# Performance work log

Measured on AMD Instinct MI355X. Metric: run time of the kernel, lower is better.

The kernel has to match this reference:

```python
import jax, jax.numpy as jnp
import numpy as np

STRIDES = (8.0, 16.0, 32.0)
SCORE_T = 0.25
NMS_T = 0.45
DET = 100          # max detections per image
PRE_NMS = 1000     # static top-k surrogate for torch.where score filtering
MAX_SIZE = 4096.0  # class offset for batched (class-aware) NMS
IMG = 640.0        # image side (square), used for box clamping
ANCHORS = np.array([[[10,13],[16,30],[33,23]],
                    [[30,61],[62,45],[59,119]],
                    [[116,90],[156,198],[373,326]]], dtype=np.float32)


def setup_inputs() -> dict:
    key = jax.random.key(0)
    k0, k1, k2 = jax.random.split(key, 3)
    return {
        "pred0": jax.random.normal(k0, (16, 80, 80, 3, 85), dtype=jnp.float32),
        "pred1": jax.random.normal(k1, (16, 40, 40, 3, 85), dtype=jnp.float32),
        "pred2": jax.random.normal(k2, (16, 20, 20, 3, 85), dtype=jnp.float32),
        "anchors": jnp.asarray(ANCHORS),
        "scale_factors": jnp.ones((16,), dtype=jnp.float32),
    }


def _decode_level(pred, stride, anc):
    # pred: [B,H,W,A,5+C], anc: [A,2]
    p = jax.nn.sigmoid(pred)
    B, H, W, A, E = p.shape
    C = E - 5
    gx, gy = jnp.meshgrid(jnp.arange(W, dtype=p.dtype),
                          jnp.arange(H, dtype=p.dtype), indexing='xy')
    grid = jnp.stack((gx, gy), -1)                      # [H,W,2] = (x,y)
    xy = (2.0 * p[..., :2] - 0.5 + grid[None, :, :, None, :]) * stride
    wh = 4.0 * jnp.square(p[..., 2:4]) * anc            # [B,H,W,A,2]
    boxes = jnp.concatenate((xy - wh * 0.5, xy + wh * 0.5), -1)  # cxcywh->xyxy
    obj = p[..., 4:5]
    s = obj * p[..., 5:]                                # [B,H,W,A,C]
    s = jnp.where((obj > SCORE_T) & (s > SCORE_T), s, 0.0)
    return boxes.reshape(B, -1, 4), s.reshape(B, -1, C)


def _box_iou_1n(box, boxes):
    # box [4], boxes [K,4] -> iou [K]
    lt = jnp.maximum(box[:2], boxes[:, :2])
    rb = jnp.minimum(box[2:], boxes[:, 2:])
    wh = jnp.clip(rb - lt, 0.0)
    inter = wh[:, 0] * wh[:, 1]
    a1 = (box[2] - box[0]) * (box[3] - box[1])
    a2 = (boxes[:, 2] - boxes[:, 0]) * (boxes[:, 3] - boxes[:, 1])
    return inter / (a1 + a2 - inter + 1e-7)


def _per_image(boxes, scores, scale):
    # boxes [M,4], scores [M,C]
    C = scores.shape[-1]
    topv, topi = jax.lax.top_k(scores.reshape(-1), PRE_NMS)
    bidx = topi // C
    lab = topi % C
    bx = boxes[bidx]                                    # [K,4]
    obx = bx + lab.astype(bx.dtype)[:, None] * MAX_SIZE  # class-offset boxes

    def body(i, st):
        sc, keep, ks = st
        j = jnp.argmax(sc)
        keep = keep.at[i].set(j)
        ks = ks.at[i].set(sc[j])
        iou = _box_iou_1n(obx[j], obx)
        sc = jnp.where(iou > NMS_T, 0.0, sc)
        return sc, keep, ks

    st0 = (topv, jnp.zeros((DET,), jnp.int32), jnp.zeros((DET,), bx.dtype))
    _, keep, ks = jax.lax.fori_loop(0, DET, body, st0)
    kb = bx[keep] / scale
    kl = lab[keep].astype(bx.dtype)
    valid = ks > 0
    kb = jnp.where(valid[:, None], kb, 0.0)
    kl = jnp.where(valid, kl, -1.0)
    return jnp.concatenate((kb, ks[:, None], kl[:, None]), -1)  # [DET,6]


def reference(pred0, pred1, pred2, anchors, scale_factors):
    preds = (pred0, pred1, pred2)
    bs, ss = [], []
    for lvl, (pred, stride) in enumerate(zip(preds, STRIDES)):
        b, s = _decode_level(pred, stride, anchors[lvl])
        bs.append(b)
        ss.append(s)
    boxes = jnp.clip(jnp.concatenate(bs, 1), 0.0, IMG)   # [B,M,4]
    scores = jnp.concatenate(ss, 1)                      # [B,M,C]
    return jax.vmap(_per_image)(boxes, scores, scale_factors)  # [B,DET,6]
```

## Files before the change

kernel.cpp:

```cpp
#include <hip/hip_runtime.h>
#include <cstdint>
#include <cstddef>

#pragma clang fp contract(off)

constexpr int NIMG  = 16;
constexpr int NB0   = 19200;
constexpr int NB1   = 4800;
constexpr int NB2   = 1200;
constexpr int NBOX  = 25200;
constexpr int NCLS  = 80;
constexpr int NCH   = 85;
constexpr int NBINS = 4096;
constexpr int CAP   = 4096;
constexpr int NTOP  = 1000;
constexpr int NDET  = 100;
constexpr float IMGSZ = 640.0f;
constexpr float BIN_SCALE = 4096.0f / 0.75f;

constexpr int TILE    = 128;
constexpr int TILES   = (NBOX + TILE - 1) / TILE;

constexpr int IOU_RPB = 40;
constexpr int LOWBIN  = 546;

typedef float float4a __attribute__((ext_vector_type(4), aligned(4)));
typedef float float2a __attribute__((ext_vector_type(2), aligned(4)));

__device__ __forceinline__ float xla_expf(float x) {
  const float kLog2e = 1.44269504088896341f;
  const float kC1 = 0.693359375f;
  const float kC2 = -2.12194440e-4f;
  const float cp0 = 1.9875691500e-4f;
  const float cp1 = 1.3981999507e-3f;
  const float cp2 = 8.3334519073e-3f;
  const float cp3 = 4.1665795894e-2f;
  const float cp4 = 1.6666665459e-1f;
  const float cp5 = 5.0000001201e-1f;
  float xc = fminf(x, 88.3762626647950f);
  xc = fmaxf(xc, -88.3762626647949f);
  float fx = floorf(fmaf(xc, kLog2e, 0.5f));
  float xr = fmaf(fx, -kC1, xc);
  xr = fmaf(fx, -kC2, xr);
  float z = xr * xr;
  float y = fmaf(cp0, xr, cp1);
  y = fmaf(y, xr, cp2);
  y = fmaf(y, xr, cp3);
  y = fmaf(y, xr, cp4);
  y = fmaf(y, xr, cp5);
  y = fmaf(y, z, xr);
  y = y + 1.0f;
  int n = (int)fx;
  float two_n = __int_as_float((n + 127) << 23);
  float r = y * two_n;
  return fmaxf(r, xc);
}

__device__ __forceinline__ float ref_sigmoid(float x) {
  return 1.0f / (1.0f + xla_expf(-x));
}

__device__ __forceinline__ float fast_sigmoid(float x) {
  float e = __expf(-x);
  return __fdividef(1.0f, 1.0f + e);
}

__device__ __forceinline__ int score_bin(float s) {
  int b = (int)((s - 0.25f) * BIN_SCALE);
  return min(max(b, 0), NBINS - 1);
}

__device__ __forceinline__ const float* locate(int img, int box,
    const float* __restrict__ p0, const float* __restrict__ p1, const float* __restrict__ p2,
    int& lvl, int& gx, int& gy, int& anc, float& stride) {
  const float* base; int r, W;
  if (box < NB0)            { lvl = 0; r = box;             W = 80; base = p0 + (size_t)img * NB0 * NCH; stride = 8.0f;  }
  else if (box < NB0 + NB1) { lvl = 1; r = box - NB0;       W = 40; base = p1 + (size_t)img * NB1 * NCH; stride = 16.0f; }
  else                      { lvl = 2; r = box - NB0 - NB1; W = 20; base = p2 + (size_t)img * NB2 * NCH; stride = 32.0f; }
  anc = r % 3;
  int cell = r / 3;
  gx = cell % W;
  gy = cell / W;
  return base + (size_t)r * NCH;
}

__device__ __forceinline__ float clip640(float v) {
  return fminf(fmaxf(v, 0.0f), IMGSZ);
}

__device__ __forceinline__ const float* row_ptr(int img, int box,
    const float* __restrict__ p0, const float* __restrict__ p1, const float* __restrict__ p2) {
  const float* base; int r;
  if (box < NB0)            { base = p0 + (size_t)img * NB0 * NCH; r = box; }
  else if (box < NB0 + NB1) { base = p1 + (size_t)img * NB1 * NCH; r = box - NB0; }
  else                      { base = p2 + (size_t)img * NB2 * NCH; r = box - NB0 - NB1; }
  return base + (size_t)r * NCH;
}

__global__ __launch_bounds__(256) void k_passA(const float* __restrict__ p0,
    const float* __restrict__ p1, const float* __restrict__ p2,
    unsigned int* __restrict__ ghist, unsigned short* __restrict__ maxbin) {
  __shared__ unsigned int hist[NBINS];
  const int tid = threadIdx.x;
  const int img  = blockIdx.x / TILES;
  const int tile = blockIdx.x % TILES;
  const int tbase = tile * TILE;
  const int nbox_tile = min(TILE, NBOX - tbase);
  const int lane = tid & 63;

  for (int i = tid; i < NBINS; i += 256) hist[i] = 0u;
  __syncthreads();

  const int b_local = tid >> 3, part = tid & 7;
  int lowc = 0;
  #pragma unroll
  for (int step = 0; step < TILE / 32; ++step) {
    int bl = step * 32 + b_local;
    bool valid = (bl < nbox_tile);
    int box = tbase + min(bl, nbox_tile - 1);
    const float* row = row_ptr(img, box, p0, p1, p2);

    float xo = row[4];
    const float* cls = row + 5 + 10 * part;
    float4a va = *(const float4a*)(cls);
    float4a vb = *(const float4a*)(cls + 4);
    float2a vc = *(const float2a*)(cls + 8);
    float v[10] = { va.x, va.y, va.z, va.w, vb.x, vb.y, vb.z, vb.w, vc.x, vc.y };

    float obj = 0.0f, tcons = 3.0e38f, thi = 3.0e38f;
    if (part == 0) {
      obj = fast_sigmoid(xo);
      if (valid && obj > 0.2499f) {
        float rr = 0.2499f / obj;
        tcons = __logf(__fdividef(rr, 1.0f - rr)) - 0.05f;
        float rh = 0.35f / obj;
        if (rh < 1.0f) thi = __logf(__fdividef(rh, 1.0f - rh)) - 0.05f;
      }
    }
    obj   = __shfl(obj,   0, 8);
    tcons = __shfl(tcons, 0, 8);
    thi   = __shfl(thi,   0, 8);

    int mb = 0;
    #pragma unroll
    for (int k = 0; k < 10; ++k) {
      float x = v[k];
      if (x > tcons) {
        if (x > thi) {
          float s = obj * fast_sigmoid(x);
          if (s > 0.2499f) {
            int bin = score_bin(s);
            atomicAdd(&hist[bin], 1u);
            mb = max(mb, bin + 1);
          }
        } else {
          ++lowc;
          mb = max(mb, LOWBIN);
        }
      }
    }
    mb = max(mb, __shfl_xor(mb, 1, 8));
    mb = max(mb, __shfl_xor(mb, 2, 8));
    mb = max(mb, __shfl_xor(mb, 4, 8));
    if (valid && part == 0)
      maxbin[(size_t)img * NBOX + tbase + bl] = (unsigned short)mb;
  }

  #pragma unroll
  for (int d = 1; d < 64; d <<= 1) lowc += __shfl_xor(lowc, d);
  if (lane == 0 && lowc) atomicAdd(&hist[0], (unsigned int)lowc);
  __syncthreads();

  for (int i = tid; i < NBINS; i += 256) {
    unsigned int v2 = hist[i];
    if (v2) atomicAdd(&ghist[img * NBINS + i], v2);
  }
}

__global__ __launch_bounds__(256) void k_thresh(const unsigned int* __restrict__ ghist,
                                                int* __restrict__ tbin) {
  __shared__ unsigned int h[NBINS];
  __shared__ unsigned int psum[256];
  const int tid = threadIdx.x;
  const int img = blockIdx.x;

  for (int i = tid; i < NBINS; i += 256) h[i] = ghist[img * NBINS + i];
  __syncthreads();
  unsigned int ps = 0;
  for (int k = 0; k < 16; ++k) ps += h[tid * 16 + k];
  psum[tid] = ps;
  __syncthreads();
  if (tid == 0) {
    long long cum = 0;
    int tb = 0;
    bool found = false;
    for (int g = 255; g >= 0 && !found; --g) {
      if (cum + (long long)psum[g] >= NTOP) {
        for (int b = g * 16 + 15; b >= g * 16; --b) {
          cum += h[b];
          if (cum >= NTOP) { tb = b; found = true; break; }
        }
      } else {
        cum += psum[g];
      }
    }
    if (!found) tb = 0;
    int tc = (tb >= 2) ? tb - 2 : 0;
    for (int b = tb - 1; b >= tc; --b) cum += h[b];
    while (cum > CAP - 8 && tc < NBINS - 1) { cum -= h[tc]; ++tc; }
    tbin[img] = tc;
  }
}

__global__ __launch_bounds__(256) void k_wlemit(const float* __restrict__ p0,
    const float* __restrict__ p1, const float* __restrict__ p2,
    const unsigned short* __restrict__ maxbin, const int* __restrict__ tbin,
    unsigned long long* __restrict__ cand, int* __restrict__ cnt) {
  __shared__ unsigned int list[256];
  __shared__ int lcnt;
  const int tid = threadIdx.x;
  const int lane = tid & 63;
  if (tid == 0) lcnt = 0;
  __syncthreads();

  int idx = blockIdx.x * 256 + tid;
  if (idx < NIMG * NBOX) {
    int img = idx / NBOX;
    int box = idx - img * NBOX;
    if ((int)maxbin[idx] > tbin[img])
      list[atomicAdd(&lcnt, 1)] = ((unsigned int)img << 16) | (unsigned int)box;
  }
  __syncthreads();
  const int n = lcnt;
  const int nsweep = (n + 31) / 32;

  for (int s = 0; s < nsweep; ++s) {
    int r = s * 32 + (tid >> 3);
    int part = tid & 7;
    bool have = (r < n);
    int img = 0, box = 0, nc = 0;
    unsigned int bm = 0;
    float obj_e = -1.0f;
    float v[10];
    if (have) {
      unsigned int e = list[r];
      img = (int)(e >> 16);
      box = (int)(e & 0xFFFFu);
      const float* row = row_ptr(img, box, p0, p1, p2);
      float xo = row[4];
      float obj_f = fast_sigmoid(xo);
      if (obj_f > 0.2499f) {
        const float* cls = row + 5 + 10 * part;
        float4a va = *(const float4a*)(cls);
        float4a vb = *(const float4a*)(cls + 4);
        float2a vc = *(const float2a*)(cls + 8);
        v[0]=va.x; v[1]=va.y; v[2]=va.z; v[3]=va.w;
        v[4]=vb.x; v[5]=vb.y; v[6]=vb.z; v[7]=vb.w;
        v[8]=vc.x; v[9]=vc.y;
        int tc = tbin[img];
        #pragma unroll
        for (int k = 0; k < 10; ++k) {
          float sf = obj_f * fast_sigmoid(v[k]);
          if (sf > 0.2499f && score_bin(sf) >= tc) {
            if (obj_e < 0.0f) obj_e = ref_sigmoid(xo);
            if (obj_e > 0.25f) {
              float se = obj_e * ref_sigmoid(v[k]);
              if (se > 0.25f) { bm |= 1u << k; ++nc; }
            }
          }
        }
      }
    }

    int mybase = 0;
    unsigned long long active = __ballot(nc > 0);
    while (active) {
      int leader = __ffsll(active) - 1;
      int limg = __shfl(img, leader);
      bool mine = (nc > 0) && (img == limg);
      unsigned long long grp = __ballot(mine);
      int incl = mine ? nc : 0;
      #pragma unroll
      for (int d = 1; d < 64; d <<= 1) {
        int t = __shfl_up(incl, d);
        if (lane >= d) incl += t;
      }
      int hi = 63 - __clzll(grp);
      int total = __shfl(incl, hi);
      int base = 0;
      if (lane == leader) base = atomicAdd(&cnt[limg], total);
      base = __shfl(base, leader);
      if (mine) mybase = base + incl - nc;
      active &= ~grp;
    }

    if (nc > 0) {
      int pos = mybase;
      #pragma unroll
      for (int k = 0; k < 10; ++k) {
        if (bm & (1u << k)) {
          float se = obj_e * ref_sigmoid(v[k]);
          if (pos < CAP) {
            unsigned int fi = (unsigned int)(box * NCLS + 10 * part + k);
            unsigned long long key =
                ((unsigned long long)__float_as_uint(se) << 32) |
                (unsigned long long)(0xFFFFFFFFu - fi);
            cand[(size_t)img * CAP + pos] = key;
          }
          ++pos;
        }
      }
    }
  }
}

#define SIDX(i) ((i) + ((i) >> 4))

__global__ __launch_bounds__(1024) void k_sort(const float* __restrict__ p0,
    const float* __restrict__ p1, const float* __restrict__ p2,
    const float* __restrict__ anchors, const unsigned long long* __restrict__ cand,
    const int* __restrict__ cnt_arr, float* __restrict__ boxes8) {
  __shared__ unsigned long long keys[CAP + CAP / 16];
  __shared__ int n2_sh, cnt_sh;
  const int tid = threadIdx.x;
  const int img = blockIdx.x;

  if (tid == 0) {
    int c = cnt_arr[img];
    c = max(0, min(c, CAP));
    int n2 = 1024;
    while (n2 < c) n2 <<= 1;
    cnt_sh = c; n2_sh = n2;
  }
  __syncthreads();
  const int cnt = cnt_sh;
  const int n2  = n2_sh;

  const unsigned long long* c = cand + (size_t)img * CAP;
  for (int i = tid; i < n2; i += 1024) keys[SIDX(i)] = (i < cnt) ? c[i] : 0ull;
  __syncthreads();

  for (int kk = 2; kk <= n2; kk <<= 1) {
    for (int j = kk >> 1; j > 0; j >>= 1) {
      for (int i = tid; i < n2; i += 1024) {
        int l = i ^ j;
        if (l > i) {
          unsigned long long a = keys[SIDX(i)], b = keys[SIDX(l)];
          bool up = ((i & kk) == 0);
          bool sw = up ? (a < b) : (a > b);
          if (sw) { keys[SIDX(i)] = b; keys[SIDX(l)] = a; }
        }
      }
      __syncthreads();
    }
  }

  float* dst = boxes8 + (size_t)img * NTOP * 8;
  if (tid < NTOP) {
    int i = tid;
    unsigned long long key = keys[SIDX(i)];
    unsigned int v = (unsigned int)(key >> 32);
    float4 fa, fb;
    if (v) {
      unsigned int idx = 0xFFFFFFFFu - (unsigned int)(key & 0xFFFFFFFFu);
      int box = (int)(idx / NCLS);
      int l   = (int)(idx % NCLS);
      int lvl, gx, gy, anc; float stride;
      const float* ptr = locate(img, box, p0, p1, p2, lvl, gx, gy, anc, stride);
      float sx = ref_sigmoid(ptr[0]);
      float sy = ref_sigmoid(ptr[1]);
      float sw = ref_sigmoid(ptr[2]);
      float sh = ref_sigmoid(ptr[3]);
      float aw = anchors[(lvl * 3 + anc) * 2 + 0];
      float ah = anchors[(lvl * 3 + anc) * 2 + 1];
      float cx = (2.0f * sx - 0.5f + (float)gx) * stride;
      float cy = (2.0f * sy - 0.5f + (float)gy) * stride;
      float ww = (4.0f * (sw * sw)) * aw;
      float hh = (4.0f * (sh * sh)) * ah;
      fa.x = clip640(cx - ww * 0.5f);
      fa.y = clip640(cy - hh * 0.5f);
      fa.z = clip640(cx + ww * 0.5f);
      fa.w = clip640(cy + hh * 0.5f);
      fb.x = __uint_as_float(v);
      fb.y = (float)l;
      fb.z = 0.0f; fb.w = 0.0f;
    } else {
      fa.x = fa.y = fa.z = fa.w = 0.0f;
      fb.x = 0.0f; fb.y = -1.0f; fb.z = 0.0f; fb.w = 0.0f;
    }
    *(float4*)(dst + i * 8)     = fa;
    *(float4*)(dst + i * 8 + 4) = fb;
  }
}

__global__ __launch_bounds__(256) void k_iou(const float* __restrict__ boxes8,
                                             unsigned int* __restrict__ mat) {
  __shared__ float obx[NTOP * 5];
  const int img = blockIdx.x / (NTOP / IOU_RPB);
  const int rg  = blockIdx.x % (NTOP / IOU_RPB);
  const float* src = boxes8 + (size_t)img * NTOP * 8;

  for (int t = threadIdx.x; t < NTOP; t += 256) {
    float4 fa = *(const float4*)(src + t * 8);
    float lab = src[t * 8 + 5];
    float off = lab * 4096.0f;
    obx[t * 5 + 0] = fa.x + off;
    obx[t * 5 + 1] = fa.y + off;
    obx[t * 5 + 2] = fa.z + off;
    obx[t * 5 + 3] = fa.w + off;
  }
  __syncthreads();

  const int wave = threadIdx.x >> 6;
  const int lane = threadIdx.x & 63;
  for (int task = wave; task < IOU_RPB * 16; task += 4) {
    int r = rg * IOU_RPB + (task >> 4);
    int w = task & 15;
    float a0 = obx[r * 5 + 0], a1 = obx[r * 5 + 1];
    float a2 = obx[r * 5 + 2], a3 = obx[r * 5 + 3];
    float areaA = (a2 - a0) * (a3 - a1);
    int col = w * 64 + lane;
    bool bit = false;
    if (col < NTOP) {
      float o0 = obx[col * 5 + 0], o1 = obx[col * 5 + 1];
      float o2 = obx[col * 5 + 2], o3 = obx[col * 5 + 3];
      float ltx = fmaxf(a0, o0);
      float lty = fmaxf(a1, o1);
      float rbx = fminf(a2, o2);
      float rby = fminf(a3, o3);
      float wx = fmaxf(rbx - ltx, 0.0f);
      float wy = fmaxf(rby - lty, 0.0f);
      float inter = wx * wy;
      float a2r = (o2 - o0) * (o3 - o1);
      float denom = areaA + a2r - inter + 1e-7f;
      bit = (inter / denom) > 0.45f;
    }
    unsigned long long m = __ballot(bit);
    if (lane == 0)
      *(unsigned long long*)(mat + ((size_t)img * NTOP + r) * 32 + w * 2) = m;
  }
}

__global__ __launch_bounds__(256) void k_nms(const unsigned int* __restrict__ mat,
    const float* __restrict__ boxes8, const float* __restrict__ scalef,
    float* __restrict__ out) {
  __shared__ uint4 mat_lds4[NTOP * 8];
  unsigned int* mat_lds = (unsigned int*)mat_lds4;
  const int tid = threadIdx.x;
  const int lane = tid & 63;
  const int img = blockIdx.x;
  const float* src = boxes8 + (size_t)img * NTOP * 8;

  const uint4* msrc = (const uint4*)(mat + (size_t)img * NTOP * 32);
  for (int i = tid; i < NTOP * 8; i += 256) mat_lds4[i] = msrc[i];
  __syncthreads();
  if (tid >= 64) return;

  unsigned int aw = 0u;
  for (int w = 0; w < 16; ++w) {
    int t = w * 64 + lane;
    float va = (t < NTOP) ? src[t * 8 + 4] : 0.0f;
    unsigned long long b = __ballot(va > 0.0f);
    if (lane == 2 * w)     aw = (unsigned int)b;
    if (lane == 2 * w + 1) aw = (unsigned int)(b >> 32);
  }
  if (lane >= 32) aw = 0u;

  int pj0 = -1, pj1 = -1;
  for (int i = 0; i < NDET; ++i) {
    unsigned long long bal = __ballot(aw != 0u);
    int j = -1;
    if (bal != 0ull) {
      int L = __ffsll(bal) - 1;
      unsigned int wL = (unsigned int)__shfl((int)aw, L);
      j = L * 32 + (__ffs(wL) - 1);
    }
    if (lane == (i & 63)) { if (i < 64) pj0 = j; else pj1 = j; }
    if (j >= 0 && lane < 32) aw &= ~mat_lds[j * 32 + lane];
  }

  const float scf = scalef[img];
  #pragma unroll
  for (int rep = 0; rep < 2; ++rep) {
    int i = rep * 64 + lane;
    if (i >= NDET) break;
    int j = (rep == 0) ? pj0 : pj1;
    float* orow = out + ((size_t)img * NDET + i) * 6;
    if (j < 0) {
      orow[0] = 0.0f; orow[1] = 0.0f; orow[2] = 0.0f;
      orow[3] = 0.0f; orow[4] = 0.0f; orow[5] = -1.0f;
    } else {
      float4 fa = *(const float4*)(src + j * 8);
      float va = src[j * 8 + 4];
      float lb = src[j * 8 + 5];
      orow[0] = fa.x / scf; orow[1] = fa.y / scf;
      orow[2] = fa.z / scf; orow[3] = fa.w / scf;
      orow[4] = va;
      orow[5] = lb;
    }
  }
}

extern "C" void kernel_launch(void* const* d_in, const int* in_sizes, int n_in,
                              void* d_out, int out_size, void* d_ws, size_t ws_size,
                              hipStream_t stream) {
  const float* p0 = (const float*)d_in[0];
  const float* p1 = (const float*)d_in[1];
  const float* p2 = (const float*)d_in[2];
  const float* anchors = (const float*)d_in[3];
  const float* scalef  = (const float*)d_in[4];
  float* out = (float*)d_out;

  char* w = (char*)d_ws;
  unsigned int* ghist = (unsigned int*)(w);
  int* cnt  = (int*)(w + 262144);
  int* tbin = (int*)(w + 262208);
  unsigned long long* cand = (unsigned long long*)(w + 262336);
  unsigned short* maxbin = (unsigned short*)(w + 262336 + 524288);
  float* boxes8 = (float*)(w + 786624 + 806400 + 64);
  unsigned int* mat = (unsigned int*)(w + 1593088 + 512000);

  hipMemsetAsync(ghist, 0, 262144 + 192, stream);

  k_passA<<<dim3(NIMG * TILES), dim3(256), 0, stream>>>(p0, p1, p2, ghist, maxbin);
  k_thresh<<<dim3(NIMG), dim3(256), 0, stream>>>(ghist, tbin);
  k_wlemit<<<dim3((NIMG * NBOX + 255) / 256), dim3(256), 0, stream>>>(p0, p1, p2, maxbin, tbin, cand, cnt);
  k_sort<<<dim3(NIMG), dim3(1024), 0, stream>>>(p0, p1, p2, anchors, cand, cnt, boxes8);
  k_iou<<<dim3(NIMG * (NTOP / IOU_RPB)), dim3(256), 0, stream>>>(boxes8, mat);
  k_nms<<<dim3(NIMG), dim3(256), 0, stream>>>(mat, boxes8, scalef, out);
}
```

Measured before the change: 180.8 us.

## Double-buffer pass-A row loads and raise the lumped low-score threshold

The histogram pass now prefetches the next step's objectness and class values into registers while the current step is processed, so global load latency overlaps with the sigmoid and binning work. Separately, the lumped low-score bin boundary moves from 546 to 2000, and the high-threshold cutoff is derived from it, so many more candidates skip the exact sigmoid and atomic histogram update and are only counted in bin 0. This relies on the downstream threshold and selection logic tolerating a much larger lumped range, and the extra register buffers raise register pressure.

```diff
diff --git a/kernel.cpp b/kernel.cpp
--- a/kernel.cpp
+++ b/kernel.cpp
@@ -22,7 +22,8 @@
 constexpr int TILES   = (NBOX + TILE - 1) / TILE;
 
 constexpr int IOU_RPB = 40;
-constexpr int LOWBIN  = 546;
+constexpr int LOWBIN  = 2000;
+constexpr float LUMP_S = 0.25f + (float)LOWBIN / BIN_SCALE;
 
 typedef float float4a __attribute__((ext_vector_type(4), aligned(4)));
 typedef float float2a __attribute__((ext_vector_type(2), aligned(4)));
@@ -113,19 +114,34 @@
 
   const int b_local = tid >> 3, part = tid & 7;
   int lowc = 0;
+
+  float   xoR[2];
+  float4a vaR[2], vbR[2];
+  float2a vcR[2];
+
+#define PA_ISSUE(SLOT, STEP) do {                                   \
+    int bl_ = (STEP) * 32 + b_local;                                \
+    int box_ = tbase + min(bl_, nbox_tile - 1);                     \
+    const float* row_ = row_ptr(img, box_, p0, p1, p2);             \
+    xoR[SLOT] = row_[4];                                            \
+    const float* cls_ = row_ + 5 + 10 * part;                       \
+    vaR[SLOT] = *(const float4a*)(cls_);                            \
+    vbR[SLOT] = *(const float4a*)(cls_ + 4);                        \
+    vcR[SLOT] = *(const float2a*)(cls_ + 8);                        \
+  } while (0)
+
+  PA_ISSUE(0, 0);
   #pragma unroll
   for (int step = 0; step < TILE / 32; ++step) {
+    const int cur = step & 1;
+    if (step + 1 < TILE / 32) PA_ISSUE((step + 1) & 1, step + 1);
+
     int bl = step * 32 + b_local;
     bool valid = (bl < nbox_tile);
-    int box = tbase + min(bl, nbox_tile - 1);
-    const float* row = row_ptr(img, box, p0, p1, p2);
-
-    float xo = row[4];
-    const float* cls = row + 5 + 10 * part;
-    float4a va = *(const float4a*)(cls);
-    float4a vb = *(const float4a*)(cls + 4);
-    float2a vc = *(const float2a*)(cls + 8);
-    float v[10] = { va.x, va.y, va.z, va.w, vb.x, vb.y, vb.z, vb.w, vc.x, vc.y };
+    float xo = xoR[cur];
+    float v[10] = { vaR[cur].x, vaR[cur].y, vaR[cur].z, vaR[cur].w,
+                    vbR[cur].x, vbR[cur].y, vbR[cur].z, vbR[cur].w,
+                    vcR[cur].x, vcR[cur].y };
 
     float obj = 0.0f, tcons = 3.0e38f, thi = 3.0e38f;
     if (part == 0) {
@@ -133,7 +149,7 @@
       if (valid && obj > 0.2499f) {
         float rr = 0.2499f / obj;
         tcons = __logf(__fdividef(rr, 1.0f - rr)) - 0.05f;
-        float rh = 0.35f / obj;
+        float rh = LUMP_S / obj;
         if (rh < 1.0f) thi = __logf(__fdividef(rh, 1.0f - rh)) - 0.05f;
       }
     }
@@ -165,6 +181,7 @@
     if (valid && part == 0)
       maxbin[(size_t)img * NBOX + tbase + bl] = (unsigned short)mb;
   }
+#undef PA_ISSUE
 
   #pragma unroll
   for (int d = 1; d < 64; d <<= 1) lowc += __shfl_xor(lowc, d);
```

New measurement: 179.4 us. No clear change (-0.7%).
